# Kernel tuning notes

Hardware: AMD Instinct MI355X
Metric: run time of the kernel (lower is better)

The kernel has to match this reference:

```python
import jax, jax.numpy as jnp
import numpy as np

D_MODEL = 2048
N_HEADS = 16
HEAD_DIM = D_MODEL // N_HEADS


def setup_inputs() -> dict:
    key = jax.random.key(0)
    k_x, k_wqkv, k_bqkv, k_wo, k_bo = jax.random.split(key, 5)
    B, T = 4, 1024
    s_in = 1.0 / np.sqrt(D_MODEL)
    return {
        "x": jax.random.normal(k_x, (B, T, D_MODEL), dtype=jnp.float32),
        "w_qkv": jax.random.uniform(k_wqkv, (D_MODEL, 3 * D_MODEL), jnp.float32, -s_in, s_in),
        "b_qkv": jax.random.uniform(k_bqkv, (3 * D_MODEL,), jnp.float32, -s_in, s_in),
        "w_out": jax.random.uniform(k_wo, (D_MODEL, D_MODEL), jnp.float32, -s_in, s_in),
        "b_out": jax.random.uniform(k_bo, (D_MODEL,), jnp.float32, -s_in, s_in),
    }


def reference(x, w_qkv, b_qkv, w_out, b_out) -> jnp.ndarray:
    B, T, C = x.shape
    qkv = x @ w_qkv + b_qkv                      # [B, T, 3C]
    q, k, v = jnp.split(qkv, 3, axis=-1)
    # [B, H, T, Dh]
    q = q.reshape(B, T, N_HEADS, HEAD_DIM).transpose(0, 2, 1, 3)
    k = k.reshape(B, T, N_HEADS, HEAD_DIM).transpose(0, 2, 1, 3)
    v = v.reshape(B, T, N_HEADS, HEAD_DIM).transpose(0, 2, 1, 3)
    scale = 1.0 / np.sqrt(HEAD_DIM).astype(np.float32)
    att = jnp.einsum("bhqd,bhkd->bhqk", q, k) * scale   # [B, H, T, T]
    causal = jnp.tril(jnp.ones((T, T), dtype=bool))
    att = jnp.where(causal, att, -jnp.inf)
    att = jax.nn.softmax(att, axis=-1)
    out = jnp.einsum("bhqk,bhkd->bhqd", att, v)          # [B, H, T, Dh]
    out = out.transpose(0, 2, 1, 3).reshape(B, T, C)
    return out @ w_out + b_out
```

## Files before the change

### kernel.cpp

```cpp
#include <hip/hip_runtime.h>
#include <hip/hip_bf16.h>
#include <math.h>

#define DM    2048
#define DQKV  6144
#define NH    16
#define DH    128
#define TT    1024
#define BB    4

typedef __bf16 bf16_t;
typedef __bf16 bf16x4 __attribute__((ext_vector_type(4)));
typedef __bf16 bf16x8 __attribute__((ext_vector_type(8)));
typedef float  f32x4  __attribute__((ext_vector_type(4)));

__device__ __forceinline__ void async16(const void* g, void* lds) {
  __builtin_amdgcn_global_load_lds(
      (const __attribute__((address_space(1))) unsigned int*)g,
      (__attribute__((address_space(3))) unsigned int*)lds, 16, 0, 0);
}

__global__ __launch_bounds__(256) void cast_kernel(const float* __restrict__ X,
                                                   bf16_t* __restrict__ Xb) {
  const size_t i = ((size_t)blockIdx.x * 256 + threadIdx.x) * 8;
  float4 a = *(const float4*)(X + i);
  float4 b = *(const float4*)(X + i + 4);
  bf16x8 o = {(bf16_t)a.x, (bf16_t)a.y, (bf16_t)a.z, (bf16_t)a.w,
              (bf16_t)b.x, (bf16_t)b.y, (bf16_t)b.z, (bf16_t)b.w};
  *(bf16x8*)(Xb + i) = o;
}

__global__ __launch_bounds__(256) void transpose_cast_kernel(
    const float* __restrict__ W, bf16_t* __restrict__ Wt, int K, int N) {
  __shared__ bf16_t tile[64][72];
  const int tid = threadIdx.x;
  const int tk = blockIdx.y * 64, tn = blockIdx.x * 64;
  {
    int r = tid >> 2, c0 = (tid & 3) * 16;
    const float* src = W + (size_t)(tk + r) * N + tn + c0;
#pragma unroll
    for (int j = 0; j < 4; ++j) {
      float4 v = *(const float4*)(src + j * 4);
      tile[r][c0 + j * 4 + 0] = (bf16_t)v.x;
      tile[r][c0 + j * 4 + 1] = (bf16_t)v.y;
      tile[r][c0 + j * 4 + 2] = (bf16_t)v.z;
      tile[r][c0 + j * 4 + 3] = (bf16_t)v.w;
    }
  }
  __syncthreads();
  {
    int n = tid >> 2, c0 = (tid & 3) * 16;
    bf16_t* dst = Wt + (size_t)(tn + n) * K + tk + c0;
#pragma unroll
    for (int j = 0; j < 4; ++j) {
      bf16x4 t = {tile[c0 + j * 4 + 0][n], tile[c0 + j * 4 + 1][n],
                  tile[c0 + j * 4 + 2][n], tile[c0 + j * 4 + 3][n]};
      *(bf16x4*)(dst + j * 4) = t;
    }
  }
}

__global__ __launch_bounds__(256) void v_transpose_kernel(
    const bf16_t* __restrict__ qkv, bf16_t* __restrict__ Vt_g) {
  __shared__ bf16_t tile[64][72];
  const int tid = threadIdx.x;
  const int dt = blockIdx.x;
  const int tt = blockIdx.y;
  const int bh = blockIdx.z;
  const int b = bh >> 4, h = bh & 15;
  {
    int r = tid >> 2, c0 = (tid & 3) * 16;
    const bf16_t* src =
        qkv + (size_t)(b * TT + tt * 64 + r) * DQKV + 2 * DM + h * DH + dt * 64 + c0;
    *(bf16x8*)&tile[r][c0]     = *(const bf16x8*)(src);
    *(bf16x8*)&tile[r][c0 + 8] = *(const bf16x8*)(src + 8);
  }
  __syncthreads();
  {
    int n = tid >> 2, c0 = (tid & 3) * 16;
    bf16_t* dst = Vt_g + (size_t)(bh * DH + dt * 64 + n) * TT + tt * 64 + c0;
#pragma unroll
    for (int j = 0; j < 4; ++j) {
      bf16x4 t = {tile[c0 + j * 4 + 0][n], tile[c0 + j * 4 + 1][n],
                  tile[c0 + j * 4 + 2][n], tile[c0 + j * 4 + 3][n]};
      *(bf16x4*)(dst + j * 4) = t;
    }
  }
}

template <bool OUT_BF16>
__global__ __launch_bounds__(256) void gemm_bt_kernel(
    const bf16_t* __restrict__ A, const bf16_t* __restrict__ Bt,
    const float* __restrict__ bias, void* __restrict__ out,
    int M, int N, int K) {
  __shared__ __align__(16) bf16_t As[128 * 64];
  __shared__ __align__(16) bf16_t Bs[128 * 64];

  const int tid  = threadIdx.x;
  const int lane = tid & 63;
  const int wave = tid >> 6;
  const int ln   = lane & 15;
  const int quad = lane >> 4;
  const int bm = blockIdx.y, bn = blockIdx.x;
  const int m0 = (wave >> 1) * 64;
  const int n0 = (wave & 1) * 64;

  const bf16_t* Abase = A + (size_t)bm * 128 * K;
  const bf16_t* Bbase = Bt + (size_t)bn * 128 * K;

  f32x4 acc[4][4] = {};

  const int kIters = K >> 6;
  for (int kt = 0; kt < kIters; ++kt) {
    __syncthreads();
#pragma unroll
    for (int j = 0; j < 4; ++j) {
      const int fb  = j * 256 + wave * 64;
      const int f   = fb + lane;
      const int row = f >> 3, c = f & 7;
      const int gc  = c ^ (row & 7);
      const size_t goff = (size_t)row * K + kt * 64 + gc * 8;
      async16(Abase + goff, (char*)As + fb * 16);
      async16(Bbase + goff, (char*)Bs + fb * 16);
    }
    __syncthreads();

#pragma unroll
    for (int ks = 0; ks < 2; ++ks) {
      bf16x8 af[4], bfr[4];
#pragma unroll
      for (int i = 0; i < 4; ++i) {
        int row = m0 + 16 * i + ln;
        int c = (ks * 4 + quad) ^ (row & 7);
        af[i] = *(const bf16x8*)((const char*)As + ((row * 8 + c) << 4));
      }
#pragma unroll
      for (int jj = 0; jj < 4; ++jj) {
        int row = n0 + 16 * jj + ln;
        int c = (ks * 4 + quad) ^ (row & 7);
        bfr[jj] = *(const bf16x8*)((const char*)Bs + ((row * 8 + c) << 4));
      }
#pragma unroll
      for (int i = 0; i < 4; ++i)
#pragma unroll
        for (int jj = 0; jj < 4; ++jj)
          acc[i][jj] = __builtin_amdgcn_mfma_f32_16x16x32_bf16(
              af[i], bfr[jj], acc[i][jj], 0, 0, 0);
    }
  }

#pragma unroll
  for (int i = 0; i < 4; ++i) {
    int rowg = bm * 128 + m0 + 16 * i + quad * 4;
#pragma unroll
    for (int j = 0; j < 4; ++j) {
      int colg = bn * 128 + n0 + 16 * j + ln;
      float bb = bias[colg];
#pragma unroll
      for (int r = 0; r < 4; ++r) {
        float val = acc[i][j][r] + bb;
        if (OUT_BF16)
          ((bf16_t*)out)[(size_t)(rowg + r) * N + colg] = (bf16_t)val;
        else
          ((float*)out)[(size_t)(rowg + r) * N + colg] = val;
      }
    }
  }
}

__global__ __launch_bounds__(256) void gemm_bt64_kernel(
    const bf16_t* __restrict__ A, const bf16_t* __restrict__ Bt,
    const float* __restrict__ bias, float* __restrict__ out,
    int M, int N, int K) {
  __shared__ __align__(16) bf16_t As[64 * 64];
  __shared__ __align__(16) bf16_t Bs[128 * 64];

  const int tid  = threadIdx.x;
  const int lane = tid & 63;
  const int wave = tid >> 6;
  const int ln   = lane & 15;
  const int quad = lane >> 4;
  const int bm = blockIdx.y, bn = blockIdx.x;
  const int m0 = (wave >> 1) * 32;
  const int n0 = (wave & 1) * 64;

  const bf16_t* Abase = A + (size_t)bm * 64 * K;
  const bf16_t* Bbase = Bt + (size_t)bn * 128 * K;

  f32x4 acc[2][4] = {};

  const int kIters = K >> 6;
  for (int kt = 0; kt < kIters; ++kt) {
    __syncthreads();
#pragma unroll
    for (int j = 0; j < 2; ++j) {
      const int fb  = j * 256 + wave * 64;
      const int f   = fb + lane;
      const int row = f >> 3, c = f & 7;
      const int gc  = c ^ (row & 7);
      async16(Abase + (size_t)row * K + kt * 64 + gc * 8, (char*)As + fb * 16);
    }
#pragma unroll
    for (int j = 0; j < 4; ++j) {
      const int fb  = j * 256 + wave * 64;
      const int f   = fb + lane;
      const int row = f >> 3, c = f & 7;
      const int gc  = c ^ (row & 7);
      async16(Bbase + (size_t)row * K + kt * 64 + gc * 8, (char*)Bs + fb * 16);
    }
    __syncthreads();

#pragma unroll
    for (int ks = 0; ks < 2; ++ks) {
      bf16x8 af[2], bfr[4];
#pragma unroll
      for (int i = 0; i < 2; ++i) {
        int row = m0 + 16 * i + ln;
        int c = (ks * 4 + quad) ^ (row & 7);
        af[i] = *(const bf16x8*)((const char*)As + ((row * 8 + c) << 4));
      }
#pragma unroll
      for (int jj = 0; jj < 4; ++jj) {
        int row = n0 + 16 * jj + ln;
        int c = (ks * 4 + quad) ^ (row & 7);
        bfr[jj] = *(const bf16x8*)((const char*)Bs + ((row * 8 + c) << 4));
      }
#pragma unroll
      for (int i = 0; i < 2; ++i)
#pragma unroll
        for (int jj = 0; jj < 4; ++jj)
          acc[i][jj] = __builtin_amdgcn_mfma_f32_16x16x32_bf16(
              af[i], bfr[jj], acc[i][jj], 0, 0, 0);
    }
  }

#pragma unroll
  for (int i = 0; i < 2; ++i) {
    int rowg = bm * 64 + m0 + 16 * i + quad * 4;
#pragma unroll
    for (int j = 0; j < 4; ++j) {
      int colg = bn * 128 + n0 + 16 * j + ln;
      float bb = bias[colg];
#pragma unroll
      for (int r = 0; r < 4; ++r)
        out[(size_t)(rowg + r) * N + colg] = acc[i][j][r] + bb;
    }
  }
}

__global__ __launch_bounds__(256, 4) void attn_kernel(
    const bf16_t* __restrict__ qkv, const bf16_t* __restrict__ Vt_g,
    bf16_t* __restrict__ attout) {
  const int bx = blockIdx.x;
  const int bh = bx & 63;
  const int qt = 15 - (bx >> 6);
  const int b  = bh >> 4;
  const int h  = bh & 15;
  const int tid  = threadIdx.x;
  const int lane = tid & 63;
  const int wave = tid >> 6;
  const int ln   = lane & 15;
  const int quad = lane >> 4;

  __shared__ __align__(16) bf16_t Ks[64 * 128];
  __shared__ __align__(16) bf16_t Vs[128 * 64];
  __shared__ __align__(16) bf16_t Ps[4 * 16 * 64];

  const float scale = 0.08838834764831845f;
  const float SHIFT = 12.0f;
  const int q0 = qt * 64 + wave * 16;

  bf16x8 aq[4];
  {
    const bf16_t* qrow = qkv + (size_t)(b * TT + q0 + ln) * DQKV + h * DH;
#pragma unroll
    for (int kt = 0; kt < 4; ++kt)
      aq[kt] = *(const bf16x8*)(qrow + kt * 32 + quad * 8);
  }

  f32x4 o[8] = {};
  float lp[4] = {0.f, 0.f, 0.f, 0.f};

  for (int c = 0; c <= qt; ++c) {
    const int kc = c * 64;
    __syncthreads();

#pragma unroll
    for (int j = 0; j < 4; ++j) {
      const int fb = j * 256 + wave * 64;
      const int l  = fb + lane;
      {
        const int row = l >> 4, cc = l & 15;
        const int gc  = cc ^ (row & 7);
        const bf16_t* g =
            qkv + (size_t)(b * TT + kc + row) * DQKV + DM + h * DH + gc * 8;
        async16(g, (char*)Ks + fb * 16);
      }
      {
        const int d = l >> 3, cc = l & 7;
        const int gc = cc ^ (d & 7);
        const bf16_t* g = Vt_g + (size_t)(bh * DH + d) * TT + kc + gc * 8;
        async16(g, (char*)Vs + fb * 16);
      }
    }
    __syncthreads();

    f32x4 sacc[4];
#pragma unroll
    for (int jt = 0; jt < 4; ++jt) {
      sacc[jt] = (f32x4){0.f, 0.f, 0.f, 0.f};
#pragma unroll
      for (int kt = 0; kt < 4; ++kt) {
        const int row = jt * 16 + ln;
        const int sc  = (kt * 4 + quad) ^ (row & 7);
        bf16x8 bk = *(const bf16x8*)((const char*)Ks + row * 256 + sc * 16);
        sacc[jt] = __builtin_amdgcn_mfma_f32_16x16x32_bf16(aq[kt], bk,
                                                           sacc[jt], 0, 0, 0);
      }
    }

    const bool diag = (c == qt);
#pragma unroll
    for (int jt = 0; jt < 4; ++jt) {
      const int colg = kc + jt * 16 + ln;
#pragma unroll
      for (int r = 0; r < 4; ++r) {
        float sv = sacc[jt][r] * scale - SHIFT;
        if (diag && colg > q0 + quad * 4 + r) sv = -1e30f;
        float pv = __expf(sv);
        lp[r] += pv;
        const int row = quad * 4 + r;
        const int col = jt * 16 + ln;
        const int sc  = (col >> 3) ^ (row & 7);
        Ps[wave * 1024 + row * 64 + sc * 8 + (col & 7)] = (bf16_t)pv;
      }
    }

#pragma unroll
    for (int ks = 0; ks < 2; ++ks) {
      const int psc = (ks * 4 + quad) ^ (ln & 7);
      bf16x8 ap =
          *(const bf16x8*)((const char*)Ps + wave * 2048 + ln * 128 + psc * 16);
#pragma unroll
      for (int nt = 0; nt < 8; ++nt) {
        const int row = nt * 16 + ln;
        const int sc  = (ks * 4 + quad) ^ (row & 7);
        bf16x8 bv = *(const bf16x8*)((const char*)Vs + row * 128 + sc * 16);
        o[nt] = __builtin_amdgcn_mfma_f32_16x16x32_bf16(ap, bv, o[nt], 0, 0, 0);
      }
    }
  }

#pragma unroll
  for (int off = 1; off < 16; off <<= 1)
#pragma unroll
    for (int r = 0; r < 4; ++r) lp[r] += __shfl_xor(lp[r], off, 64);

#pragma unroll
  for (int r = 0; r < 4; ++r) {
    float inv = 1.0f / lp[r];
    int t = q0 + quad * 4 + r;
    bf16_t* orow = attout + (size_t)(b * TT + t) * DM + h * DH;
#pragma unroll
    for (int nt = 0; nt < 8; ++nt)
      orow[nt * 16 + ln] = (bf16_t)(o[nt][r] * inv);
  }
}

extern "C" void kernel_launch(void* const* d_in, const int* in_sizes, int n_in,
                              void* d_out, int out_size, void* d_ws,
                              size_t ws_size, hipStream_t stream) {
  const float* x     = (const float*)d_in[0];
  const float* w_qkv = (const float*)d_in[1];
  const float* b_qkv = (const float*)d_in[2];
  const float* w_out = (const float*)d_in[3];
  const float* b_out = (const float*)d_in[4];
  float* out = (float*)d_out;

  char* ws = (char*)d_ws;
  bf16_t* qkv    = (bf16_t*)(ws);
  bf16_t* wqkv_t = (bf16_t*)(ws + 50331648);
  bf16_t* Vt_g   = wqkv_t;
  bf16_t* wout_t = (bf16_t*)(ws + 75497472);
  bf16_t* xb     = (bf16_t*)(ws + 83886080);
  bf16_t* attout = xb;

  dim3 blk(256);
  cast_kernel<<<dim3(4096), blk, 0, stream>>>(x, xb);
  transpose_cast_kernel<<<dim3(96, 32), blk, 0, stream>>>(w_qkv, wqkv_t, 2048, 6144);
  transpose_cast_kernel<<<dim3(32, 32), blk, 0, stream>>>(w_out, wout_t, 2048, 2048);
  gemm_bt_kernel<true>
      <<<dim3(48, 32), blk, 0, stream>>>(xb, wqkv_t, b_qkv, qkv, 4096, 6144, 2048);
  v_transpose_kernel<<<dim3(2, 16, 64), blk, 0, stream>>>(qkv, Vt_g);
  attn_kernel<<<dim3(1024), blk, 0, stream>>>(qkv, Vt_g, attout);
  gemm_bt64_kernel
      <<<dim3(16, 64), blk, 0, stream>>>(attout, wout_t, b_out, out, 4096, 2048, 2048);
}
```

Measured before the change: 350.0 us.

## Rewrite QKV GEMM with 256x192 tiles, double-buffered async loads, XCD swizzle

Replaces the 128x128 single-buffered QKV projection GEMM with a 512-thread kernel using 256x192 block tiles, a two-stage double-buffered LDS pipeline with manual vmcnt waits, and interleaved async loads between MFMA phases under raised wave priority. It also remaps block indices so neighbouring tiles land on the same XCD for L2 reuse. The aim is to hide global-load latency and raise arithmetic intensity per block. In exchange it uses more LDS and registers, which limits occupancy, and it relies on hand-placed waitcnt values staying correct.

Measured after the change: 339.4 us. 3.0% less time.

```diff
diff --git a/kernel.cpp b/kernel.cpp
--- a/kernel.cpp
+++ b/kernel.cpp
@@ -18,6 +18,12 @@
   __builtin_amdgcn_global_load_lds(
       (const __attribute__((address_space(1))) unsigned int*)g,
       (__attribute__((address_space(3))) unsigned int*)lds, 16, 0, 0);
+}
+
+__device__ __forceinline__ void block_barrier() {
+  asm volatile("" ::: "memory");
+  __builtin_amdgcn_s_barrier();
+  asm volatile("" ::: "memory");
 }
 
 __global__ __launch_bounds__(256) void cast_kernel(const float* __restrict__ X,
@@ -88,74 +94,124 @@
   }
 }
 
+#define GBM 256
+#define GBN 192
 template <bool OUT_BF16>
-__global__ __launch_bounds__(256) void gemm_bt_kernel(
+__global__ __launch_bounds__(512, 2) void gemm_big_kernel(
     const bf16_t* __restrict__ A, const bf16_t* __restrict__ Bt,
     const float* __restrict__ bias, void* __restrict__ out,
-    int M, int N, int K) {
-  __shared__ __align__(16) bf16_t As[128 * 64];
-  __shared__ __align__(16) bf16_t Bs[128 * 64];
+    int M, int N, int K, int nbm) {
+  __shared__ __align__(16) bf16_t As[2][GBM * 64];
+  __shared__ __align__(16) bf16_t Bs[2][GBN * 64];
 
   const int tid  = threadIdx.x;
   const int lane = tid & 63;
   const int wave = tid >> 6;
   const int ln   = lane & 15;
   const int quad = lane >> 4;
-  const int bm = blockIdx.y, bn = blockIdx.x;
-  const int m0 = (wave >> 1) * 64;
-  const int n0 = (wave & 1) * 64;
-
-  const bf16_t* Abase = A + (size_t)bm * 128 * K;
-  const bf16_t* Bbase = Bt + (size_t)bn * 128 * K;
-
-  f32x4 acc[4][4] = {};
-
-  const int kIters = K >> 6;
-  for (int kt = 0; kt < kIters; ++kt) {
-    __syncthreads();
-#pragma unroll
-    for (int j = 0; j < 4; ++j) {
-      const int fb  = j * 256 + wave * 64;
+
+  const int cpx = gridDim.x >> 3;
+  const int wg  = (blockIdx.x & 7) * cpx + (blockIdx.x >> 3);
+  const int bm  = wg & (nbm - 1);
+  const int bn  = wg / nbm;
+
+  const bf16_t* Abase = A + (size_t)bm * GBM * K;
+  const bf16_t* Bbase = Bt + (size_t)bn * GBN * K;
+
+  const int m0 = (wave >> 2) * 128;
+  const int n0 = (wave & 3) * 48;
+
+  f32x4 acc[8][3] = {};
+
+  const int NT = K >> 6;
+
+  auto stageA = [&](int kt, int d) {
+#pragma unroll
+    for (int s = 0; s < 4; ++s) {
+      const int fb  = s * 512 + wave * 64;
       const int f   = fb + lane;
       const int row = f >> 3, c = f & 7;
       const int gc  = c ^ (row & 7);
-      const size_t goff = (size_t)row * K + kt * 64 + gc * 8;
-      async16(Abase + goff, (char*)As + fb * 16);
-      async16(Bbase + goff, (char*)Bs + fb * 16);
-    }
-    __syncthreads();
-
+      async16(Abase + (size_t)row * K + kt * 64 + gc * 8,
+              (char*)(&As[d][0]) + fb * 16);
+    }
+  };
+  auto stageB = [&](int kt, int d) {
+#pragma unroll
+    for (int s = 0; s < 3; ++s) {
+      const int fb  = s * 512 + wave * 64;
+      const int f   = fb + lane;
+      const int row = f >> 3, c = f & 7;
+      const int gc  = c ^ (row & 7);
+      async16(Bbase + (size_t)row * K + kt * 64 + gc * 8,
+              (char*)(&Bs[d][0]) + fb * 16);
+    }
+  };
+
+  stageA(0, 0);
+  stageB(0, 0);
+  stageA(1, 1);
+  stageB(1, 1);
+  asm volatile("s_waitcnt vmcnt(7)" ::: "memory");
+  block_barrier();
+
+  for (int kt = 0; kt < NT; ++kt) {
+    const int cur = kt & 1;
+
+    bf16x8 af[8][2], bfr[3][2];
 #pragma unroll
     for (int ks = 0; ks < 2; ++ks) {
-      bf16x8 af[4], bfr[4];
-#pragma unroll
-      for (int i = 0; i < 4; ++i) {
-        int row = m0 + 16 * i + ln;
-        int c = (ks * 4 + quad) ^ (row & 7);
-        af[i] = *(const bf16x8*)((const char*)As + ((row * 8 + c) << 4));
-      }
-#pragma unroll
-      for (int jj = 0; jj < 4; ++jj) {
-        int row = n0 + 16 * jj + ln;
-        int c = (ks * 4 + quad) ^ (row & 7);
-        bfr[jj] = *(const bf16x8*)((const char*)Bs + ((row * 8 + c) << 4));
-      }
-#pragma unroll
-      for (int i = 0; i < 4; ++i)
-#pragma unroll
-        for (int jj = 0; jj < 4; ++jj)
-          acc[i][jj] = __builtin_amdgcn_mfma_f32_16x16x32_bf16(
-              af[i], bfr[jj], acc[i][jj], 0, 0, 0);
-    }
-  }
-
-#pragma unroll
-  for (int i = 0; i < 4; ++i) {
-    int rowg = bm * 128 + m0 + 16 * i + quad * 4;
-#pragma unroll
-    for (int j = 0; j < 4; ++j) {
-      int colg = bn * 128 + n0 + 16 * j + ln;
-      float bb = bias[colg];
+#pragma unroll
+      for (int i = 0; i < 8; ++i) {
+        const int row = m0 + 16 * i + ln;
+        const int c = (ks * 4 + quad) ^ (row & 7);
+        af[i][ks] =
+            *(const bf16x8*)((const char*)(&As[cur][0]) + ((row * 8 + c) << 4));
+      }
+#pragma unroll
+      for (int j = 0; j < 3; ++j) {
+        const int row = n0 + 16 * j + ln;
+        const int c = (ks * 4 + quad) ^ (row & 7);
+        bfr[j][ks] =
+            *(const bf16x8*)((const char*)(&Bs[cur][0]) + ((row * 8 + c) << 4));
+      }
+    }
+    asm volatile("s_waitcnt lgkmcnt(0)" ::: "memory");
+    block_barrier();
+
+    if (kt + 2 < NT) stageA(kt + 2, cur);
+    __builtin_amdgcn_s_setprio(1);
+#pragma unroll
+    for (int i = 0; i < 8; ++i)
+#pragma unroll
+      for (int j = 0; j < 3; ++j)
+        acc[i][j] = __builtin_amdgcn_mfma_f32_16x16x32_bf16(af[i][0], bfr[j][0],
+                                                            acc[i][j], 0, 0, 0);
+    __builtin_amdgcn_s_setprio(0);
+    if (kt + 2 < NT) stageB(kt + 2, cur);
+    __builtin_amdgcn_s_setprio(1);
+#pragma unroll
+    for (int i = 0; i < 8; ++i)
+#pragma unroll
+      for (int j = 0; j < 3; ++j)
+        acc[i][j] = __builtin_amdgcn_mfma_f32_16x16x32_bf16(af[i][1], bfr[j][1],
+                                                            acc[i][j], 0, 0, 0);
+    __builtin_amdgcn_s_setprio(0);
+
+    if (kt + 2 < NT)
+      asm volatile("s_waitcnt vmcnt(7)" ::: "memory");
+    else
+      asm volatile("s_waitcnt vmcnt(0)" ::: "memory");
+    block_barrier();
+  }
+
+#pragma unroll
+  for (int i = 0; i < 8; ++i) {
+    const int rowg = bm * GBM + m0 + 16 * i + quad * 4;
+#pragma unroll
+    for (int j = 0; j < 3; ++j) {
+      const int colg = bn * GBN + n0 + 16 * j + ln;
+      const float bb = bias[colg];
 #pragma unroll
       for (int r = 0; r < 4; ++r) {
         float val = acc[i][j][r] + bb;
@@ -389,8 +445,8 @@
   cast_kernel<<<dim3(4096), blk, 0, stream>>>(x, xb);
   transpose_cast_kernel<<<dim3(96, 32), blk, 0, stream>>>(w_qkv, wqkv_t, 2048, 6144);
   transpose_cast_kernel<<<dim3(32, 32), blk, 0, stream>>>(w_out, wout_t, 2048, 2048);
-  gemm_bt_kernel<true>
-      <<<dim3(48, 32), blk, 0, stream>>>(xb, wqkv_t, b_qkv, qkv, 4096, 6144, 2048);
+  gemm_big_kernel<true><<<dim3(512), dim3(512), 0, stream>>>(
+      xb, wqkv_t, b_qkv, qkv, 4096, 6144, 2048, 16);
   v_transpose_kernel<<<dim3(2, 16, 64), blk, 0, stream>>>(qkv, Vt_g);
   attn_kernel<<<dim3(1024), blk, 0, stream>>>(qkv, Vt_g, attout);
   gemm_bt64_kernel
```
